# Optimization experiments

Hardware: AMD Instinct MI355X
Metric: run time of the kernel (lower is better)

## Reference

```python
import jax, jax.numpy as jnp
import numpy as np

FEAT = 256
HID = 256
HEADS = 4
DH = HID // HEADS
SCALE = DH ** (-0.5)


def _linear(x, W, b):
    # torch nn.Linear convention: W is [out, in]
    return jnp.einsum('...i,oi->...o', x, W) + b


def _layernorm(x, gamma, beta, eps=1e-5):
    mu = jnp.mean(x, axis=-1, keepdims=True)
    var = jnp.mean(jnp.square(x - mu), axis=-1, keepdims=True)
    return (x - mu) * jax.lax.rsqrt(var + eps) * gamma + beta


def setup_inputs() -> dict:
    key = jax.random.key(0)
    ks = jax.random.split(key, 16)
    B, N = 4, 2048
    def w(k, shape, fan_in):
        return jax.random.uniform(k, shape, jnp.float32, -1.0, 1.0) / np.sqrt(fan_in)
    return {
        'x0': jax.random.normal(ks[0], (B, N, FEAT), jnp.float32),
        'x1': jax.random.normal(ks[1], (B, N, FEAT), jnp.float32),
        'Wqk': w(ks[2], (HID, FEAT), FEAT), 'bqk': w(ks[3], (HID,), FEAT),
        'Wv': w(ks[4], (HID, FEAT), FEAT), 'bv': w(ks[5], (HID,), FEAT),
        'Wp': w(ks[6], (HID, HID), HID), 'bp': w(ks[7], (HID,), HID),
        'W1': w(ks[8], (FEAT * 2, FEAT + HID), FEAT + HID), 'b1': w(ks[9], (FEAT * 2,), FEAT + HID),
        'gamma': jnp.ones((FEAT * 2,), jnp.float32), 'beta': jnp.zeros((FEAT * 2,), jnp.float32),
        'W2': w(ks[10], (FEAT, FEAT * 2), FEAT * 2), 'b2': w(ks[11], (FEAT,), FEAT * 2),
    }


def _forward(x0, x1, Wqk, bqk, Wv, bv, Wp, bp, W1, b1, gamma, beta, W2, b2):
    B, N0, _ = x0.shape
    N1 = x1.shape[1]

    def heads(t):  # [B, N, HID] -> [B, H, N, DH]
        return t.reshape(t.shape[0], t.shape[1], HEADS, DH).transpose(0, 2, 1, 3)

    qk0 = heads(_linear(x0, Wqk, bqk)) * (SCALE ** 0.5)
    qk1 = heads(_linear(x1, Wqk, bqk)) * (SCALE ** 0.5)
    v0 = heads(_linear(x0, Wv, bv))
    v1 = heads(_linear(x1, Wv, bv))

    sim = jnp.einsum('bhid,bhjd->bhij', qk0, qk1)  # [B,H,N0,N1]
    attn01 = jax.nn.softmax(sim, axis=-1)                      # rows over N1
    attn10 = jax.nn.softmax(sim.transpose(0, 1, 3, 2), axis=-1)  # [B,H,N1,N0], rows over N0

    m0 = jnp.einsum('bhij,bhjd->bhid', attn01, v1)  # [B,H,N0,DH]
    m1 = jnp.einsum('bhij,bhjd->bhid', attn10, v0)  # [B,H,N1,DH]

    def merge(t):  # [B,H,N,DH] -> [B,N,HID]
        return t.transpose(0, 2, 1, 3).reshape(t.shape[0], t.shape[2], HID)

    m0 = _linear(merge(m0), Wp, bp)
    m1 = _linear(merge(m1), Wp, bp)

    def mlp(x, m):
        h = _linear(jnp.concatenate([x, m], axis=-1), W1, b1)
        h = jax.nn.gelu(_layernorm(h, gamma, beta), approximate=False)
        return x + _linear(h, W2, b2)

    return mlp(x0, m0), mlp(x1, m1)


def reference(x0, x1, Wqk, bqk, Wv, bv, Wp, bp, W1, b1, gamma, beta, W2, b2):
    return _forward(x0, x1, Wqk, bqk, Wv, bv, Wp, bp, W1, b1, gamma, beta, W2, b2)
```

## Files before the change

### kernel.cpp

```cpp
#include <hip/hip_runtime.h>
#include <hip/hip_bf16.h>
#include <math.h>

typedef __hip_bfloat16 hbf;
typedef __attribute__((ext_vector_type(8))) short short8;
typedef __attribute__((ext_vector_type(4))) short short4v;
typedef __attribute__((ext_vector_type(4))) float f32x4;

#define ROWS 8192
#define SQSL 0.4246609001440095f

__device__ __forceinline__ short f2b(float f) {
    union { hbf h; short s; } u; u.h = __float2bfloat16(f); return u.s;
}
__device__ __forceinline__ float b2f(short s) {
    union { unsigned u; float f; } x;
    x.u = ((unsigned)(unsigned short)s) << 16; return x.f;
}

__global__ __launch_bounds__(256)
void prep_w(const float* __restrict__ Wqk, const float* __restrict__ Wv,
            short* __restrict__ wq, short* __restrict__ wv)
{
    const int bid = blockIdx.x, tid = threadIdx.x;
    const float* src; short* dst; int base; float sc = 1.f;
    if (bid < 64) { src = Wqk; dst = wq; base = bid;      sc = SQSL; }
    else          { src = Wv;  dst = wv; base = bid - 64; }
    int i = base * 256 + tid;
    float4 f = ((const float4*)src)[i];
    short4v s;
    s[0] = f2b(f.x * sc); s[1] = f2b(f.y * sc);
    s[2] = f2b(f.z * sc); s[3] = f2b(f.w * sc);
    *(short4v*)(dst + (size_t)i * 4) = s;
}

__device__ void prep_big(int bid, int tid,
                         const float* __restrict__ Wp, const float* __restrict__ W1,
                         const float* __restrict__ W2, const float* __restrict__ bp,
                         const float* __restrict__ b1,
                         short* __restrict__ w1c, short* __restrict__ w2,
                         float* __restrict__ bc)
{
    if (bid < 384) {
        int i = (bid - 128) * 256 + tid;
        int n = i >> 7, c = (i & 127) * 4;
        if (c < 256) {
            float4 f = ((const float4*)W1)[i];
            short4v s;
            s[0] = f2b(f.x); s[1] = f2b(f.y); s[2] = f2b(f.z); s[3] = f2b(f.w);
            *(short4v*)(w1c + (size_t)n * 512 + c) = s;
        }
    } else if (bid < 512) {
        int i = (bid - 384) * 256 + tid;
        float4 f = ((const float4*)W2)[i];
        short4v s;
        s[0] = f2b(f.x); s[1] = f2b(f.y); s[2] = f2b(f.z); s[3] = f2b(f.w);
        *(short4v*)(w2 + (size_t)i * 4) = s;
    } else if (bid < 1024) {
        int n = bid - 512;
        const float* wrow = W1 + (size_t)n * 512 + 256;
        float acc = 0.f;
        for (int k = 0; k < 256; ++k)
            acc += wrow[k] * Wp[(size_t)k * 256 + tid];
        w1c[(size_t)n * 512 + 256 + tid] = f2b(acc);
    } else {
        int n = (bid - 1024) * 256 + tid;
        const float* wrow = W1 + (size_t)n * 512 + 256;
        float acc = b1[n];
        for (int k = 0; k < 256; ++k) acc += wrow[k] * bp[k];
        bc[n] = acc;
    }
}

__global__ __launch_bounds__(256)
void gemm_qkv(const float* __restrict__ x0, const float* __restrict__ x1,
              const short* __restrict__ Wa, const short* __restrict__ Wb,
              const float* __restrict__ bias0, const float* __restrict__ bias1,
              short* __restrict__ qkb, short* __restrict__ vtb,
              const float* __restrict__ Wp, const float* __restrict__ W1,
              const float* __restrict__ W2f, const float* __restrict__ bpv,
              const float* __restrict__ b1,
              short* __restrict__ w1c, short* __restrict__ w2c,
              float* __restrict__ bc)
{
    const int bid = blockIdx.x;
    const int tid = threadIdx.x;
    if (bid >= 1024) {
        prep_big(bid - 1024 + 128, tid, Wp, W1, W2f, bpv, b1, w1c, w2c, bc);
        return;
    }
    const int fid  = bid;
    const int col0 = (fid >> 8) * 128;
    const int row0 = (fid & 255) * 64;
    const int lane = tid & 63, wave = tid >> 6;
    const int ln = lane & 15, quad = lane >> 4;
    const int wm = wave & 1, wn = wave >> 1;

    __shared__ short smem[64 * 72 + 128 * 72];
    short* As = smem;
    short* Bs = smem + 64 * 72;
    short* Vt = smem;

    const int ar = tid >> 2, ac = tid & 3;

    f32x4 acc[2][4];
    #pragma unroll
    for (int i = 0; i < 2; ++i)
        #pragma unroll
        for (int j = 0; j < 4; ++j) acc[i][j] = {0.f, 0.f, 0.f, 0.f};

    const short* wbase = (col0 < 256) ? Wa + (size_t)col0 * 256
                                      : Wb + (size_t)(col0 - 256) * 256;
    const float* xrow = (row0 + ar < ROWS)
        ? x0 + (size_t)(row0 + ar) * 256
        : x1 + (size_t)(row0 + ar - ROWS) * 256;

    float4 aF[4];
    short8 bR[4];
    #pragma unroll
    for (int i = 0; i < 4; ++i) aF[i] = ((const float4*)(xrow + ac * 16))[i];
    bR[0] = *(const short8*)(wbase + (size_t)ar * 256 + ac * 16);
    bR[1] = *(const short8*)(wbase + (size_t)ar * 256 + ac * 16 + 8);
    bR[2] = *(const short8*)(wbase + (size_t)(ar + 64) * 256 + ac * 16);
    bR[3] = *(const short8*)(wbase + (size_t)(ar + 64) * 256 + ac * 16 + 8);

    for (int k0 = 0; k0 < 256; k0 += 64) {
        {
            short8 s0, s1;
            s0[0] = f2b(aF[0].x); s0[1] = f2b(aF[0].y); s0[2] = f2b(aF[0].z); s0[3] = f2b(aF[0].w);
            s0[4] = f2b(aF[1].x); s0[5] = f2b(aF[1].y); s0[6] = f2b(aF[1].z); s0[7] = f2b(aF[1].w);
            s1[0] = f2b(aF[2].x); s1[1] = f2b(aF[2].y); s1[2] = f2b(aF[2].z); s1[3] = f2b(aF[2].w);
            s1[4] = f2b(aF[3].x); s1[5] = f2b(aF[3].y); s1[6] = f2b(aF[3].z); s1[7] = f2b(aF[3].w);
            *(short8*)&As[ar * 72 + ac * 16]     = s0;
            *(short8*)&As[ar * 72 + ac * 16 + 8] = s1;
        }
        *(short8*)&Bs[ar * 72 + ac * 16]            = bR[0];
        *(short8*)&Bs[ar * 72 + ac * 16 + 8]        = bR[1];
        *(short8*)&Bs[(ar + 64) * 72 + ac * 16]     = bR[2];
        *(short8*)&Bs[(ar + 64) * 72 + ac * 16 + 8] = bR[3];
        __syncthreads();

        if (k0 + 64 < 256) {
            const int kk = k0 + 64 + ac * 16;
            #pragma unroll
            for (int i = 0; i < 4; ++i) aF[i] = ((const float4*)(xrow + kk))[i];
            bR[0] = *(const short8*)(wbase + (size_t)ar * 256 + kk);
            bR[1] = *(const short8*)(wbase + (size_t)ar * 256 + kk + 8);
            bR[2] = *(const short8*)(wbase + (size_t)(ar + 64) * 256 + kk);
            bR[3] = *(const short8*)(wbase + (size_t)(ar + 64) * 256 + kk + 8);
        }

        short8 a[2][2], b[4][2];
        #pragma unroll
        for (int mi = 0; mi < 2; ++mi)
            #pragma unroll
            for (int ks = 0; ks < 2; ++ks)
                a[mi][ks] = *(const short8*)&As[(wm * 32 + mi * 16 + ln) * 72 + ks * 32 + quad * 8];
        #pragma unroll
        for (int nj = 0; nj < 4; ++nj)
            #pragma unroll
            for (int ks = 0; ks < 2; ++ks)
                b[nj][ks] = *(const short8*)&Bs[(wn * 64 + nj * 16 + ln) * 72 + ks * 32 + quad * 8];
        #pragma unroll
        for (int mi = 0; mi < 2; ++mi)
            #pragma unroll
            for (int nj = 0; nj < 4; ++nj) {
                acc[mi][nj] = __builtin_amdgcn_mfma_f32_16x16x32_bf16(
                                  b[nj][0], a[mi][0], acc[mi][nj], 0, 0, 0);
                acc[mi][nj] = __builtin_amdgcn_mfma_f32_16x16x32_bf16(
                                  b[nj][1], a[mi][1], acc[mi][nj], 0, 0, 0);
            }
        __syncthreads();
    }

    if (col0 < 256) {
        #pragma unroll
        for (int nj = 0; nj < 4; ++nj) {
            const int wcol = col0 + wn * 64 + nj * 16 + quad * 4;
            float4 bb = *(const float4*)(bias0 + wcol);
            #pragma unroll
            for (int mi = 0; mi < 2; ++mi) {
                const int tok = row0 + wm * 32 + mi * 16 + ln;
                f32x4 v = acc[mi][nj];
                short4v o;
                o[0] = f2b(fmaf(bb.x, SQSL, v[0]));
                o[1] = f2b(fmaf(bb.y, SQSL, v[1]));
                o[2] = f2b(fmaf(bb.z, SQSL, v[2]));
                o[3] = f2b(fmaf(bb.w, SQSL, v[3]));
                *(short4v*)(qkb + (size_t)tok * 256 + wcol) = o;
            }
        }
    } else {
        #pragma unroll
        for (int nj = 0; nj < 4; ++nj) {
            const int wrel = wn * 64 + nj * 16 + quad * 4;
            float4 bb = *(const float4*)(bias1 + (col0 - 256) + wrel);
            #pragma unroll
            for (int mi = 0; mi < 2; ++mi) {
                const int tl = wm * 32 + mi * 16 + ln;
                f32x4 v = acc[mi][nj];
                Vt[(wrel + 0) * 72 + tl] = f2b(v[0] + bb.x);
                Vt[(wrel + 1) * 72 + tl] = f2b(v[1] + bb.y);
                Vt[(wrel + 2) * 72 + tl] = f2b(v[2] + bb.z);
                Vt[(wrel + 3) * 72 + tl] = f2b(v[3] + bb.w);
            }
        }
        __syncthreads();
        {
            const int g4 = (row0 >> 11) * 4, tc0 = row0 & 2047;
            const int r = tid >> 1, hf = tid & 1;
            const int vcol = (col0 - 256) + r;
            const int hh = vcol >> 6, d = vcol & 63;
            short* dst = vtb + (size_t)((g4 + hh) * 64 + d) * 2048 + tc0 + hf * 32;
            #pragma unroll
            for (int cc = 0; cc < 4; ++cc)
                *(short8*)(dst + cc * 8) = *(const short8*)&Vt[r * 72 + hf * 32 + cc * 8];
        }
    }
}

__global__ __launch_bounds__(128, 2)
void attn8(const short* __restrict__ qkb, const short* __restrict__ vtbuf,
           short* __restrict__ pO0, short* __restrict__ pO1,
           float* __restrict__ l0, float* __restrict__ l1)
{
    const int nfl = blockIdx.x + (blockIdx.y << 4) + (blockIdx.z << 8);
    const int qt  = nfl >> 6;
    const int gg  = nfl & 63;
    const int b    = (gg >> 2) & 3, h = gg & 3;
    const int dir  = gg >> 5;
    const int half = (gg >> 4) & 1;
    const int tid = threadIdx.x;
    const int lane = tid & 63, wave = tid >> 6;
    const int ln   = lane & 15, quad = lane >> 4;

    const int qbase = dir * ROWS + b * 2048;
    const int kbase = (1 - dir) * ROWS + b * 2048;
    const int vg    = ((1 - dir) * 4 + b) * 4 + h;
    const int jlo   = half * 1024, jhi = jlo + 1024;

    short* __restrict__ pO = half ? pO1 : pO0;
    float* __restrict__ lb = half ? l1  : l0;

    __shared__ short QP[128 * 72];
    __shared__ short KS[64 * 72];
    __shared__ short VT[64 * 72];

    const int c = tid & 7, r0 = tid >> 3;

    short8 qf[4][2];
    #pragma unroll
    for (int mi = 0; mi < 4; ++mi)
        #pragma unroll
        for (int ks = 0; ks < 2; ++ks)
            qf[mi][ks] = *(const short8*)(
                qkb + (size_t)(qbase + qt * 128 + wave * 64 + mi * 16 + ln) * 256
                + h * 64 + ks * 32 + quad * 8);

    #pragma unroll
    for (int g = 0; g < 4; ++g) {
        int r = r0 + g * 16;
        *(short8*)&KS[r * 72 + c * 8] =
            *(const short8*)(qkb + (size_t)(kbase + jlo + r) * 256 + h * 64 + c * 8);
        *(short8*)&VT[r * 72 + c * 8] =
            *(const short8*)(vtbuf + (size_t)(vg * 64 + r) * 2048 + jlo + c * 8);
    }
    __syncthreads();

    short8 ones;
    #pragma unroll
    for (int j = 0; j < 8; ++j) ones[j] = (short)0x3F80;

    f32x4 Ot[4][4];
    #pragma unroll
    for (int mi = 0; mi < 4; ++mi)
        #pragma unroll
        for (int dt = 0; dt < 4; ++dt) Ot[mi][dt] = {0.f, 0.f, 0.f, 0.f};
    f32x4 lacc[4];
    #pragma unroll
    for (int mi = 0; mi < 4; ++mi) lacc[mi] = {0.f, 0.f, 0.f, 0.f};

    for (int j0 = jlo; j0 < jhi; j0 += 64) {
        short8 kreg[4], vreg[4];
        const bool more = (j0 + 64) < jhi;
        if (more) {
            #pragma unroll
            for (int g = 0; g < 4; ++g) {
                int r = r0 + g * 16;
                kreg[g] = *(const short8*)(qkb + (size_t)(kbase + j0 + 64 + r) * 256
                                           + h * 64 + c * 8);
                vreg[g] = *(const short8*)(vtbuf + (size_t)(vg * 64 + r) * 2048
                                           + j0 + 64 + c * 8);
            }
        }

        f32x4 St[4][4];
        #pragma unroll
        for (int t = 0; t < 4; ++t) {
            short8 k0 = *(const short8*)&KS[(t * 16 + ln) * 72 + quad * 8];
            short8 k1 = *(const short8*)&KS[(t * 16 + ln) * 72 + 32 + quad * 8];
            #pragma unroll
            for (int mi = 0; mi < 4; ++mi) {
                f32x4 z = {0.f, 0.f, 0.f, 0.f};
                z = __builtin_amdgcn_mfma_f32_16x16x32_bf16(k0, qf[mi][0], z, 0, 0, 0);
                St[mi][t] = __builtin_amdgcn_mfma_f32_16x16x32_bf16(k1, qf[mi][1], z, 0, 0, 0);
            }
        }

        #pragma unroll
        for (int mi = 0; mi < 4; ++mi)
            #pragma unroll
            for (int t = 0; t < 4; ++t) {
                float p0 = __builtin_amdgcn_exp2f(St[mi][t][0]);
                float p1 = __builtin_amdgcn_exp2f(St[mi][t][1]);
                float p2 = __builtin_amdgcn_exp2f(St[mi][t][2]);
                float p3 = __builtin_amdgcn_exp2f(St[mi][t][3]);
                unsigned d0 = __builtin_amdgcn_perm(__float_as_uint(p1),
                                                    __float_as_uint(p0), 0x07060302u);
                unsigned d1 = __builtin_amdgcn_perm(__float_as_uint(p3),
                                                    __float_as_uint(p2), 0x07060302u);
                *(int2*)&QP[(wave * 64 + mi * 16 + ln) * 72 + t * 16 + quad * 4] =
                    make_int2((int)d0, (int)d1);
            }

        short8 pa[4][2];
        #pragma unroll
        for (int mi = 0; mi < 4; ++mi)
            #pragma unroll
            for (int ks = 0; ks < 2; ++ks)
                pa[mi][ks] = *(const short8*)&QP[(wave * 64 + mi * 16 + ln) * 72
                                                 + ks * 32 + quad * 8];
        #pragma unroll
        for (int mi = 0; mi < 4; ++mi) {
            lacc[mi] = __builtin_amdgcn_mfma_f32_16x16x32_bf16(
                           ones, pa[mi][0], lacc[mi], 0, 0, 0);
            lacc[mi] = __builtin_amdgcn_mfma_f32_16x16x32_bf16(
                           ones, pa[mi][1], lacc[mi], 0, 0, 0);
        }
        #pragma unroll
        for (int dt = 0; dt < 4; ++dt) {
            short8 v0 = *(const short8*)&VT[(dt * 16 + ln) * 72 + quad * 8];
            short8 v1 = *(const short8*)&VT[(dt * 16 + ln) * 72 + 32 + quad * 8];
            #pragma unroll
            for (int mi = 0; mi < 4; ++mi) {
                Ot[mi][dt] = __builtin_amdgcn_mfma_f32_16x16x32_bf16(
                                 v0, pa[mi][0], Ot[mi][dt], 0, 0, 0);
                Ot[mi][dt] = __builtin_amdgcn_mfma_f32_16x16x32_bf16(
                                 v1, pa[mi][1], Ot[mi][dt], 0, 0, 0);
            }
        }
        __syncthreads();

        if (more) {
            #pragma unroll
            for (int g = 0; g < 4; ++g) {
                int r = r0 + g * 16;
                *(short8*)&KS[r * 72 + c * 8] = kreg[g];
                *(short8*)&VT[r * 72 + c * 8] = vreg[g];
            }
        }
        __syncthreads();
    }

    #pragma unroll
    for (int mi = 0; mi < 4; ++mi) {
        int tok = qbase + qt * 128 + wave * 64 + mi * 16 + ln;
        if (quad == 0) lb[tok] = lacc[mi][0];
        #pragma unroll
        for (int dt = 0; dt < 4; ++dt) {
            short4v o;
            #pragma unroll
            for (int r = 0; r < 4; ++r) o[r] = f2b(Ot[mi][dt][r]);
            *(short4v*)(pO + (size_t)tok * 256 + h * 64 + dt * 16 + quad * 4) = o;
        }
    }
}

__global__ __launch_bounds__(256)
void mlp_fused(const float* __restrict__ x0, const float* __restrict__ x1,
               const short* __restrict__ pO0, const short* __restrict__ pO1,
               const float* __restrict__ l0, const float* __restrict__ l1,
               const short* __restrict__ w1c, const short* __restrict__ w2,
               const float* __restrict__ bc, const float* __restrict__ gamma,
               const float* __restrict__ beta, const float* __restrict__ b2,
               float* __restrict__ out)
{
    const int tok0 = blockIdx.x * 32;
    const int tid = threadIdx.x;
    const int lane = tid & 63, wave = tid >> 6;
    const int ln = lane & 15, quad = lane >> 4;

    __shared__ short H [32 * 520];
    __shared__ short Bs[256 * 72];
    __shared__ float stats[4][2][32];

    const int br = tid >> 2, bq = tid & 3;
    short8 bp[8];
    auto loadB = [&](const short* W, int rw, int k0) {
        const short* src = W + (size_t)(rw + br) * 512 + k0 + bq * 16;
        #pragma unroll
        for (int q = 0; q < 4; ++q) {
            bp[2 * q]     = *(const short8*)(src + (size_t)q * 64 * 512);
            bp[2 * q + 1] = *(const short8*)(src + (size_t)q * 64 * 512 + 8);
        }
    };
    loadB(w1c, 0, 0);

    {
        const int arow = tid >> 3, ac = tid & 7;
        const int tok = tok0 + arow;
        if (ac < 4) {
            const float* xr = (tok < ROWS ? x0 + (size_t)tok * 256
                                          : x1 + (size_t)(tok - ROWS) * 256) + ac * 64;
            #pragma unroll
            for (int cc = 0; cc < 8; ++cc) {
                float4 f0 = ((const float4*)(xr + cc * 8))[0];
                float4 f1 = ((const float4*)(xr + cc * 8))[1];
                short8 s;
                s[0] = f2b(f0.x); s[1] = f2b(f0.y); s[2] = f2b(f0.z); s[3] = f2b(f0.w);
                s[4] = f2b(f1.x); s[5] = f2b(f1.y); s[6] = f2b(f1.z); s[7] = f2b(f1.w);
                *(short8*)&H[arow * 520 + ac * 64 + cc * 8] = s;
            }
        } else {
            const int vc = (ac - 4) * 64;
            const float inv = __builtin_amdgcn_rcpf(l0[tok] + l1[tok]);
            #pragma unroll
            for (int cc = 0; cc < 8; ++cc) {
                short8 a = *(const short8*)(pO0 + (size_t)tok * 256 + vc + cc * 8);
                short8 b = *(const short8*)(pO1 + (size_t)tok * 256 + vc + cc * 8);
                short8 s;
                #pragma unroll
                for (int j = 0; j < 8; ++j)
                    s[j] = f2b((b2f(a[j]) + b2f(b[j])) * inv);
                *(short8*)&H[arow * 520 + 256 + vc + cc * 8] = s;
            }
        }
    }

    f32x4 acc[2][8];
    #pragma unroll
    for (int i = 0; i < 2; ++i)
        #pragma unroll
        for (int j = 0; j < 8; ++j) acc[i][j] = {0.f, 0.f, 0.f, 0.f};

    __syncthreads();

    for (int k2 = 0; k2 < 8; ++k2) {
        const int k0 = k2 * 64;
        short8 a0[2], a1[2];
        #pragma unroll
        for (int ks = 0; ks < 2; ++ks) {
            a0[ks] = *(const short8*)&H[ln * 520 + k0 + ks * 32 + quad * 8];
            a1[ks] = *(const short8*)&H[(16 + ln) * 520 + k0 + ks * 32 + quad * 8];
        }
        #pragma unroll
        for (int p = 0; p < 2; ++p) {
            #pragma unroll
            for (int q = 0; q < 4; ++q) {
                *(short8*)&Bs[(br + q * 64) * 72 + bq * 16]     = bp[2 * q];
                *(short8*)&Bs[(br + q * 64) * 72 + bq * 16 + 8] = bp[2 * q + 1];
            }
            __syncthreads();
            if (p == 0)          loadB(w1c, 256, k0);
            else if (k2 < 7)     loadB(w1c, 0, k0 + 64);
            #pragma unroll
            for (int nj = 0; nj < 4; ++nj) {
                #pragma unroll
                for (int ks = 0; ks < 2; ++ks) {
                    short8 bf = *(const short8*)&Bs[(wave * 64 + nj * 16 + ln) * 72
                                                    + ks * 32 + quad * 8];
                    acc[0][p * 4 + nj] = __builtin_amdgcn_mfma_f32_16x16x32_bf16(
                                             bf, a0[ks], acc[0][p * 4 + nj], 0, 0, 0);
                    acc[1][p * 4 + nj] = __builtin_amdgcn_mfma_f32_16x16x32_bf16(
                                             bf, a1[ks], acc[1][p * 4 + nj], 0, 0, 0);
                }
            }
            __syncthreads();
        }
    }

    loadB(w2, 0, 0);

    #pragma unroll
    for (int p = 0; p < 2; ++p)
        #pragma unroll
        for (int nj = 0; nj < 4; ++nj) {
            int hcol = p * 256 + wave * 64 + nj * 16 + quad * 4;
            float4 bb = *(const float4*)(bc + hcol);
            acc[0][p * 4 + nj][0] += bb.x; acc[1][p * 4 + nj][0] += bb.x;
            acc[0][p * 4 + nj][1] += bb.y; acc[1][p * 4 + nj][1] += bb.y;
            acc[0][p * 4 + nj][2] += bb.z; acc[1][p * 4 + nj][2] += bb.z;
            acc[0][p * 4 + nj][3] += bb.w; acc[1][p * 4 + nj][3] += bb.w;
        }

    #pragma unroll
    for (int mi = 0; mi < 2; ++mi) {
        float s1 = 0.f, s2 = 0.f;
        #pragma unroll
        for (int j = 0; j < 8; ++j)
            #pragma unroll
            for (int r = 0; r < 4; ++r) {
                float v = acc[mi][j][r];
                s1 += v; s2 += v * v;
            }
        s1 += __shfl_xor(s1, 16); s2 += __shfl_xor(s2, 16);
        s1 += __shfl_xor(s1, 32); s2 += __shfl_xor(s2, 32);
        if (quad == 0) {
            stats[wave][0][mi * 16 + ln] = s1;
            stats[wave][1][mi * 16 + ln] = s2;
        }
    }
    __syncthreads();

    float mean[2], rstd[2];
    #pragma unroll
    for (int mi = 0; mi < 2; ++mi) {
        int t = mi * 16 + ln;
        float s1 = stats[0][0][t] + stats[1][0][t] + stats[2][0][t] + stats[3][0][t];
        float s2 = stats[0][1][t] + stats[1][1][t] + stats[2][1][t] + stats[3][1][t];
        mean[mi] = s1 * (1.f / 512.f);
        float var = s2 * (1.f / 512.f) - mean[mi] * mean[mi];
        rstd[mi] = rsqrtf(var + 1e-5f);
    }

    #pragma unroll
    for (int p = 0; p < 2; ++p)
        #pragma unroll
        for (int nj = 0; nj < 4; ++nj) {
            int hcol = p * 256 + wave * 64 + nj * 16 + quad * 4;
            float4 gm = *(const float4*)(gamma + hcol);
            float4 bt = *(const float4*)(beta + hcol);
            #pragma unroll
            for (int mi = 0; mi < 2; ++mi) {
                short4v o;
                #pragma unroll
                for (int r = 0; r < 4; ++r) {
                    float g = (r == 0) ? gm.x : (r == 1) ? gm.y : (r == 2) ? gm.z : gm.w;
                    float bta = (r == 0) ? bt.x : (r == 1) ? bt.y : (r == 2) ? bt.z : bt.w;
                    float y = (acc[mi][p * 4 + nj][r] - mean[mi]) * rstd[mi] * g + bta;
                    float u = y * fmaf(y * y, 0.0356774081f, 0.7978845608f);
                    float e = __builtin_amdgcn_exp2f(u * -2.8853900818f);
                    o[r] = f2b(y * __builtin_amdgcn_rcpf(1.f + e));
                }
                *(short4v*)&H[(mi * 16 + ln) * 520 + hcol] = o;
            }
        }

    f32x4 acc2[2][4];
    #pragma unroll
    for (int i = 0; i < 2; ++i)
        #pragma unroll
        for (int j = 0; j < 4; ++j) acc2[i][j] = {0.f, 0.f, 0.f, 0.f};

    for (int s = 0; s < 8; ++s) {
        const int k0 = s * 64;
        #pragma unroll
        for (int q = 0; q < 4; ++q) {
            *(short8*)&Bs[(br + q * 64) * 72 + bq * 16]     = bp[2 * q];
            *(short8*)&Bs[(br + q * 64) * 72 + bq * 16 + 8] = bp[2 * q + 1];
        }
        __syncthreads();
        if (s < 7) loadB(w2, 0, k0 + 64);
        short8 h0[2], h1[2];
        #pragma unroll
        for (int ks = 0; ks < 2; ++ks) {
            h0[ks] = *(const short8*)&H[ln * 520 + k0 + ks * 32 + quad * 8];
            h1[ks] = *(const short8*)&H[(16 + ln) * 520 + k0 + ks * 32 + quad * 8];
        }
        #pragma unroll
        for (int nj = 0; nj < 4; ++nj) {
            #pragma unroll
            for (int ks = 0; ks < 2; ++ks) {
                short8 wf = *(const short8*)&Bs[(wave * 64 + nj * 16 + ln) * 72
                                                + ks * 32 + quad * 8];
                acc2[0][nj] = __builtin_amdgcn_mfma_f32_16x16x32_bf16(
                                  wf, h0[ks], acc2[0][nj], 0, 0, 0);
                acc2[1][nj] = __builtin_amdgcn_mfma_f32_16x16x32_bf16(
                                  wf, h1[ks], acc2[1][nj], 0, 0, 0);
            }
        }
        __syncthreads();
    }

    #pragma unroll
    for (int nj = 0; nj < 4; ++nj) {
        int ocol = wave * 64 + nj * 16 + quad * 4;
        float4 bb = *(const float4*)(b2 + ocol);
        #pragma unroll
        for (int mi = 0; mi < 2; ++mi) {
            int tok = tok0 + mi * 16 + ln;
            const float* xr = (tok < ROWS ? x0 + (size_t)tok * 256
                                          : x1 + (size_t)(tok - ROWS) * 256);
            float4 rv = *(const float4*)(xr + ocol);
            float4 o;
            o.x = acc2[mi][nj][0] + bb.x + rv.x;
            o.y = acc2[mi][nj][1] + bb.y + rv.y;
            o.z = acc2[mi][nj][2] + bb.z + rv.z;
            o.w = acc2[mi][nj][3] + bb.w + rv.w;
            *(float4*)(out + (size_t)tok * 256 + ocol) = o;
        }
    }
}

extern "C" void kernel_launch(void* const* d_in, const int* in_sizes, int n_in,
                              void* d_out, int out_size, void* d_ws, size_t ws_size,
                              hipStream_t stream)
{
    const float* x0    = (const float*)d_in[0];
    const float* x1    = (const float*)d_in[1];
    const float* Wqk   = (const float*)d_in[2];
    const float* bqk   = (const float*)d_in[3];
    const float* Wv    = (const float*)d_in[4];
    const float* bv    = (const float*)d_in[5];
    const float* Wp    = (const float*)d_in[6];
    const float* bp    = (const float*)d_in[7];
    const float* W1    = (const float*)d_in[8];
    const float* b1    = (const float*)d_in[9];
    const float* gamma = (const float*)d_in[10];
    const float* beta  = (const float*)d_in[11];
    const float* W2    = (const float*)d_in[12];
    const float* b2    = (const float*)d_in[13];
    float* out = (float*)d_out;

    char* ws = (char*)d_ws;
    const size_t MB = 1024 * 1024;
    short* qkb  = (short*)ws;
    short* vtb  = (short*)(ws + 8  * MB);
    short* pO0  = (short*)(ws + 16 * MB);
    short* pO1  = (short*)(ws + 24 * MB);
    float* l0   = (float*)(ws + 32 * MB);
    float* l1   = l0 + 16384;
    float* bc   = l1 + 16384;
    short* wq   = (short*)(bc + 512);
    short* wv   = wq + 65536;
    short* w1c  = wv + 65536;
    short* w2   = w1c + 262144;

    prep_w<<<128, 256, 0, stream>>>(Wqk, Wv, wq, wv);
    gemm_qkv<<<1922, 256, 0, stream>>>(x0, x1, wq, wv, bqk, bv, qkb, vtb,
                                       Wp, W1, W2, bp, b1, w1c, w2, bc);
    attn8<<<dim3(16, 16, 4), 128, 0, stream>>>(qkb, vtb, pO0, pO1, l0, l1);
    mlp_fused<<<512, 256, 0, stream>>>(x0, x1, pO0, pO1, l0, l1, w1c, w2, bc,
                                       gamma, beta, b2, out);
}
```

Baseline: 193.6 us.

## Double MLP block tile to 64 tokens with 8 waves in 2x4 grid

The fused MLP kernel now processes 64 tokens per block with 512 threads. The waves are arranged as 2 row groups by 4 column groups, so each staged weight tile in LDS is reused across twice as many tokens. Weight global loads are split across more threads, each holding half as many prefetch registers. The grid halves to 256 blocks and LDS per block roughly doubles for the H buffer. This may reduce per-CU concurrency or leave the workload imbalanced across CUs.

```diff
diff --git a/kernel.cpp b/kernel.cpp
--- a/kernel.cpp
+++ b/kernel.cpp
@@ -376,7 +376,7 @@
     }
 }
 
-__global__ __launch_bounds__(256)
+__global__ __launch_bounds__(512, 2)
 void mlp_fused(const float* __restrict__ x0, const float* __restrict__ x1,
                const short* __restrict__ pO0, const short* __restrict__ pO1,
                const float* __restrict__ l0, const float* __restrict__ l1,
@@ -385,24 +385,30 @@
                const float* __restrict__ beta, const float* __restrict__ b2,
                float* __restrict__ out)
 {
-    const int tok0 = blockIdx.x * 32;
+    const int tok0 = blockIdx.x * 64;
     const int tid = threadIdx.x;
     const int lane = tid & 63, wave = tid >> 6;
     const int ln = lane & 15, quad = lane >> 4;
-
-    __shared__ short H [32 * 520];
+    const int wm = wave >> 2, wn = wave & 3;
+
+    __shared__ short H [64 * 520];
     __shared__ short Bs[256 * 72];
-    __shared__ float stats[4][2][32];
+    __shared__ float stats[4][2][64];
 
     const int br = tid >> 2, bq = tid & 3;
-    short8 bp[8];
+    short8 bp4[4];
     auto loadB = [&](const short* W, int rw, int k0) {
         const short* src = W + (size_t)(rw + br) * 512 + k0 + bq * 16;
-        #pragma unroll
-        for (int q = 0; q < 4; ++q) {
-            bp[2 * q]     = *(const short8*)(src + (size_t)q * 64 * 512);
-            bp[2 * q + 1] = *(const short8*)(src + (size_t)q * 64 * 512 + 8);
-        }
+        bp4[0] = *(const short8*)(src);
+        bp4[1] = *(const short8*)(src + 8);
+        bp4[2] = *(const short8*)(src + (size_t)128 * 512);
+        bp4[3] = *(const short8*)(src + (size_t)128 * 512 + 8);
+    };
+    auto stageB = [&]() {
+        *(short8*)&Bs[br * 72 + bq * 16]             = bp4[0];
+        *(short8*)&Bs[br * 72 + bq * 16 + 8]         = bp4[1];
+        *(short8*)&Bs[(br + 128) * 72 + bq * 16]     = bp4[2];
+        *(short8*)&Bs[(br + 128) * 72 + bq * 16 + 8] = bp4[3];
     };
     loadB(w1c, 0, 0);
 
@@ -450,16 +456,12 @@
         short8 a0[2], a1[2];
         #pragma unroll
         for (int ks = 0; ks < 2; ++ks) {
-            a0[ks] = *(const short8*)&H[ln * 520 + k0 + ks * 32 + quad * 8];
-            a1[ks] = *(const short8*)&H[(16 + ln) * 520 + k0 + ks * 32 + quad * 8];
+            a0[ks] = *(const short8*)&H[(wm * 32 + ln) * 520 + k0 + ks * 32 + quad * 8];
+            a1[ks] = *(const short8*)&H[(wm * 32 + 16 + ln) * 520 + k0 + ks * 32 + quad * 8];
         }
         #pragma unroll
         for (int p = 0; p < 2; ++p) {
-            #pragma unroll
-            for (int q = 0; q < 4; ++q) {
-                *(short8*)&Bs[(br + q * 64) * 72 + bq * 16]     = bp[2 * q];
-                *(short8*)&Bs[(br + q * 64) * 72 + bq * 16 + 8] = bp[2 * q + 1];
-            }
+            stageB();
             __syncthreads();
             if (p == 0)          loadB(w1c, 256, k0);
             else if (k2 < 7)     loadB(w1c, 0, k0 + 64);
@@ -467,7 +469,7 @@
             for (int nj = 0; nj < 4; ++nj) {
                 #pragma unroll
                 for (int ks = 0; ks < 2; ++ks) {
-                    short8 bf = *(const short8*)&Bs[(wave * 64 + nj * 16 + ln) * 72
+                    short8 bf = *(const short8*)&Bs[(wn * 64 + nj * 16 + ln) * 72
                                                     + ks * 32 + quad * 8];
                     acc[0][p * 4 + nj] = __builtin_amdgcn_mfma_f32_16x16x32_bf16(
                                              bf, a0[ks], acc[0][p * 4 + nj], 0, 0, 0);
@@ -485,7 +487,7 @@
     for (int p = 0; p < 2; ++p)
         #pragma unroll
         for (int nj = 0; nj < 4; ++nj) {
-            int hcol = p * 256 + wave * 64 + nj * 16 + quad * 4;
+            int hcol = p * 256 + wn * 64 + nj * 16 + quad * 4;
             float4 bb = *(const float4*)(bc + hcol);
             acc[0][p * 4 + nj][0] += bb.x; acc[1][p * 4 + nj][0] += bb.x;
             acc[0][p * 4 + nj][1] += bb.y; acc[1][p * 4 + nj][1] += bb.y;
@@ -506,8 +508,8 @@
         s1 += __shfl_xor(s1, 16); s2 += __shfl_xor(s2, 16);
         s1 += __shfl_xor(s1, 32); s2 += __shfl_xor(s2, 32);
         if (quad == 0) {
-            stats[wave][0][mi * 16 + ln] = s1;
-            stats[wave][1][mi * 16 + ln] = s2;
+            stats[wn][0][wm * 32 + mi * 16 + ln] = s1;
+            stats[wn][1][wm * 32 + mi * 16 + ln] = s2;
         }
     }
     __syncthreads();
@@ -515,7 +517,7 @@
     float mean[2], rstd[2];
     #pragma unroll
     for (int mi = 0; mi < 2; ++mi) {
-        int t = mi * 16 + ln;
+        int t = wm * 32 + mi * 16 + ln;
         float s1 = stats[0][0][t] + stats[1][0][t] + stats[2][0][t] + stats[3][0][t];
         float s2 = stats[0][1][t] + stats[1][1][t] + stats[2][1][t] + stats[3][1][t];
         mean[mi] = s1 * (1.f / 512.f);
@@ -527,7 +529,7 @@
     for (int p = 0; p < 2; ++p)
         #pragma unroll
         for (int nj = 0; nj < 4; ++nj) {
-            int hcol = p * 256 + wave * 64 + nj * 16 + quad * 4;
+            int hcol = p * 256 + wn * 64 + nj * 16 + quad * 4;
             float4 gm = *(const float4*)(gamma + hcol);
             float4 bt = *(const float4*)(beta + hcol);
             #pragma unroll
@@ -542,7 +544,7 @@
                     float e = __builtin_amdgcn_exp2f(u * -2.8853900818f);
                     o[r] = f2b(y * __builtin_amdgcn_rcpf(1.f + e));
                 }
-                *(short4v*)&H[(mi * 16 + ln) * 520 + hcol] = o;
+                *(short4v*)&H[(wm * 32 + mi * 16 + ln) * 520 + hcol] = o;
             }
         }
 
@@ -554,24 +556,20 @@
 
     for (int s = 0; s < 8; ++s) {
         const int k0 = s * 64;
-        #pragma unroll
-        for (int q = 0; q < 4; ++q) {
-            *(short8*)&Bs[(br + q * 64) * 72 + bq * 16]     = bp[2 * q];
-            *(short8*)&Bs[(br + q * 64) * 72 + bq * 16 + 8] = bp[2 * q + 1];
-        }
+        stageB();
         __syncthreads();
         if (s < 7) loadB(w2, 0, k0 + 64);
         short8 h0[2], h1[2];
         #pragma unroll
         for (int ks = 0; ks < 2; ++ks) {
-            h0[ks] = *(const short8*)&H[ln * 520 + k0 + ks * 32 + quad * 8];
-            h1[ks] = *(const short8*)&H[(16 + ln) * 520 + k0 + ks * 32 + quad * 8];
+            h0[ks] = *(const short8*)&H[(wm * 32 + ln) * 520 + k0 + ks * 32 + quad * 8];
+            h1[ks] = *(const short8*)&H[(wm * 32 + 16 + ln) * 520 + k0 + ks * 32 + quad * 8];
         }
         #pragma unroll
         for (int nj = 0; nj < 4; ++nj) {
             #pragma unroll
             for (int ks = 0; ks < 2; ++ks) {
-                short8 wf = *(const short8*)&Bs[(wave * 64 + nj * 16 + ln) * 72
+                short8 wf = *(const short8*)&Bs[(wn * 64 + nj * 16 + ln) * 72
                                                 + ks * 32 + quad * 8];
                 acc2[0][nj] = __builtin_amdgcn_mfma_f32_16x16x32_bf16(
                                   wf, h0[ks], acc2[0][nj], 0, 0, 0);
@@ -584,11 +582,11 @@
 
     #pragma unroll
     for (int nj = 0; nj < 4; ++nj) {
-        int ocol = wave * 64 + nj * 16 + quad * 4;
+        int ocol = wn * 64 + nj * 16 + quad * 4;
         float4 bb = *(const float4*)(b2 + ocol);
         #pragma unroll
         for (int mi = 0; mi < 2; ++mi) {
-            int tok = tok0 + mi * 16 + ln;
+            int tok = tok0 + wm * 32 + mi * 16 + ln;
             const float* xr = (tok < ROWS ? x0 + (size_t)tok * 256
                                           : x1 + (size_t)(tok - ROWS) * 256);
             float4 rv = *(const float4*)(xr + ocol);
@@ -640,6 +638,6 @@
     gemm_qkv<<<1922, 256, 0, stream>>>(x0, x1, wq, wv, bqk, bv, qkb, vtb,
                                        Wp, W1, W2, bp, b1, w1c, w2, bc);
     attn8<<<dim3(16, 16, 4), 128, 0, stream>>>(qkb, vtb, pO0, pO1, l0, l1);
-    mlp_fused<<<512, 256, 0, stream>>>(x0, x1, pO0, pO1, l0, l1, w1c, w2, bc,
+    mlp_fused<<<256, 512, 0, stream>>>(x0, x1, pO0, pO1, l0, l1, w1c, w2, bc,
                                        gamma, beta, b2, out);
 }
```

Result: no change. 193.5 us (-0.1%).
